# Optimization experiments

Measured on AMD Instinct MI355X. Metric: run time of the kernel, lower is better.

Reference implementation:

```python
import jax, jax.numpy as jnp
import numpy as np

N = 30000
E = 480000
F_IN = 100
HID = 64
HEADS = 4
NCLS = 47
HC = HEADS * HID  # 256
NEG_SLOPE = 0.2
BN_EPS = 1e-5


def setup_inputs() -> dict:
    key = jax.random.key(0)
    ks = jax.random.split(key, 32)
    s = 0.1
    inp = {
        'x': jax.random.normal(ks[0], (N, F_IN), jnp.float32),
        'edge_index': jax.random.randint(ks[1], (2, E), 0, N, jnp.int32),
        # layer 0: GATConv(F_IN -> HID, heads, concat=True)
        'w0': jax.random.normal(ks[2], (F_IN, HC), jnp.float32) * s,
        'as0': jax.random.normal(ks[3], (HEADS, HID), jnp.float32) * s,
        'ad0': jax.random.normal(ks[4], (HEADS, HID), jnp.float32) * s,
        'b0': jnp.zeros((HC,), jnp.float32),
        'sw0': jax.random.normal(ks[5], (F_IN, HC), jnp.float32) * s,
        'sb0': jnp.zeros((HC,), jnp.float32),
        'g0': jnp.ones((HC,), jnp.float32),
        'be0': jnp.zeros((HC,), jnp.float32),
        # layer 1: GATConv(HC -> HID, heads, concat=True)
        'w1': jax.random.normal(ks[6], (HC, HC), jnp.float32) * s,
        'as1': jax.random.normal(ks[7], (HEADS, HID), jnp.float32) * s,
        'ad1': jax.random.normal(ks[8], (HEADS, HID), jnp.float32) * s,
        'b1': jnp.zeros((HC,), jnp.float32),
        'sw1': jax.random.normal(ks[9], (HC, HC), jnp.float32) * s,
        'sb1': jnp.zeros((HC,), jnp.float32),
        'g1': jnp.ones((HC,), jnp.float32),
        'be1': jnp.zeros((HC,), jnp.float32),
        # layer 2: GATConv(HC -> NCLS, heads, concat=False)
        'w2': jax.random.normal(ks[10], (HC, HEADS * NCLS), jnp.float32) * s,
        'as2': jax.random.normal(ks[11], (HEADS, NCLS), jnp.float32) * s,
        'ad2': jax.random.normal(ks[12], (HEADS, NCLS), jnp.float32) * s,
        'b2': jnp.zeros((NCLS,), jnp.float32),
        'sw2': jax.random.normal(ks[13], (HC, NCLS), jnp.float32) * s,
        'sb2': jnp.zeros((NCLS,), jnp.float32),
    }
    return inp


def gat_conv(x, src, dst, W, a_src, a_dst, bias, heads, out_ch, concat):
    # shared linear for src/dst (PyG GATConv with int in_channels)
    h = (x @ W).reshape(N, heads, out_ch)           # [N,H,C]
    al_s = jnp.sum(h * a_src, axis=-1)              # [N,H]
    al_d = jnp.sum(h * a_dst, axis=-1)              # [N,H]
    e = jax.nn.leaky_relu(al_s[src] + al_d[dst], NEG_SLOPE)  # [E,H]
    # segment (per-destination) softmax
    m = jax.ops.segment_max(e, dst, num_segments=N)
    e = jnp.exp(e - m[dst])
    den = jax.ops.segment_sum(e, dst, num_segments=N)
    alpha = e / (den[dst] + 1e-16)                  # [E,H]
    msg = h[src] * alpha[:, :, None]                # [E,H,C]
    out = jax.ops.segment_sum(msg, dst, num_segments=N)  # [N,H,C]
    out = out.reshape(N, heads * out_ch) if concat else out.mean(axis=1)
    return out + bias


def batch_norm(x, gamma, beta):
    mu = jnp.mean(x, axis=0)
    var = jnp.var(x, axis=0)
    return gamma * (x - mu) * jax.lax.rsqrt(var + BN_EPS) + beta


def reference(x, edge_index, w0, as0, ad0, b0, sw0, sb0, g0, be0,
              w1, as1, ad1, b1, sw1, sb1, g1, be1,
              w2, as2, ad2, b2, sw2, sb2):
    src, dst = edge_index[0], edge_index[1]
    # layer 0
    h = gat_conv(x, src, dst, w0, as0, ad0, b0, HEADS, HID, True)
    h = h + x @ sw0 + sb0
    h = jax.nn.elu(batch_norm(h, g0, be0))
    # layer 1
    h2 = gat_conv(h, src, dst, w1, as1, ad1, b1, HEADS, HID, True)
    h2 = h2 + h @ sw1 + sb1
    h2 = jax.nn.elu(batch_norm(h2, g1, be1))
    # layer 2 (concat=False -> mean over heads)
    out = gat_conv(h2, src, dst, w2, as2, ad2, b2, HEADS, NCLS, False)
    out = out + h2 @ sw2 + sb2
    return jax.nn.log_softmax(out, axis=-1)
```

## Files before the change

### kernel.cpp

```cpp
#include <hip/hip_runtime.h>
#include <math.h>

#define NN 30000
#define EE 480000
#define FIN 100
#define NCLS 47
#define NCOPY 16
#define SCAN_B 118

typedef unsigned short ushortt;
typedef __attribute__((ext_vector_type(8))) short bf16x8;
typedef __attribute__((ext_vector_type(8))) unsigned short us8;
typedef __attribute__((ext_vector_type(4))) float f32x4;
typedef __attribute__((ext_vector_type(2))) float f32x2;

__device__ unsigned char g_H8[(size_t)NN * 256];
__device__ ushortt g_Sb[(size_t)NN * 256];
__device__ float   g_S2[(size_t)NN * 48];
__device__ ushortt g_Fb[(size_t)NN * 256];
__device__ ushortt g_Xb[(size_t)NN * 128];
__device__ ushortt g_Wc0[512 * 128];
__device__ ushortt g_Wc1[512 * 256];
__device__ ushortt g_Wc2[235 * 256];
__device__ float g_als[NN * 4];
__device__ float g_ald[NN * 4];
__device__ int   g_rowptr[NN + 1];
__device__ int   g_counts[NN];
__device__ int   g_cur[NN];
__device__ int   g_bsum[128];
__device__ int   g_esrc[EE];
__device__ float g_stat[2 * NCOPY * 512];

__device__ __forceinline__ float wsum(float v) {
#pragma unroll
  for (int o = 32; o > 0; o >>= 1) v += __shfl_xor(v, o, 64);
  return v;
}
__device__ __forceinline__ float lrelu(float x) { return x > 0.f ? x : 0.2f * x; }
__device__ __forceinline__ ushortt f2bf(float f) {
  unsigned int u = __float_as_uint(f);
  unsigned int r = u + 0x7FFF + ((u >> 16) & 1);
  return (ushortt)(r >> 16);
}
__device__ __forceinline__ float bf2f(ushortt u) {
  return __uint_as_float(((unsigned int)u) << 16);
}
__device__ __forceinline__ unsigned int pk4_fp8(float f0, float f1, float f2, float f3) {
  unsigned int r = 0;
  r = __builtin_amdgcn_cvt_pk_fp8_f32(f0, f1, r, false);
  r = __builtin_amdgcn_cvt_pk_fp8_f32(f2, f3, r, true);
  return r;
}
__device__ __forceinline__ int swz(int row, int k) {
  return (k & ~63) | ((((k >> 3) & 7) ^ (row & 7)) << 3) | (k & 7);
}
__device__ __forceinline__ void glds16(const ushortt* gp, ushortt* lp) {
  __builtin_amdgcn_global_load_lds(
      (const __attribute__((address_space(1))) unsigned int*)gp,
      (__attribute__((address_space(3))) unsigned int*)lp, 16, 0, 0);
}

#define CW0 (512 * 128)
#define CW1 (512 * 256)
#define CW2 (235 * 256)
#define STATZ (2 * NCOPY * 512)
__global__ void conv_kernel(const float* __restrict__ w0, const float* __restrict__ sw0,
                            const float* __restrict__ w1, const float* __restrict__ sw1,
                            const float* __restrict__ w2, const float* __restrict__ sw2,
                            const float* __restrict__ x, const int* __restrict__ dst) {
  int i = blockIdx.x * blockDim.x + threadIdx.x;
  if (i < CW0) {
    int m = i >> 7, k = i & 127;
    float v = 0.f;
    if (k < FIN) v = (m < 256) ? w0[k * 256 + m] : sw0[k * 256 + (m - 256)];
    g_Wc0[(m << 7) | swz(m, k)] = f2bf(v);
    return;
  }
  i -= CW0;
  if (i < CW1) {
    int m = i >> 8, k = i & 255;
    float v = (m < 256) ? w1[k * 256 + m] : sw1[k * 256 + (m - 256)];
    g_Wc1[(m << 8) | swz(m, k)] = f2bf(v);
    return;
  }
  i -= CW1;
  if (i < CW2) {
    int m = i >> 8, k = i & 255;
    float v = (m < 188) ? w2[(size_t)k * 188 + m] : sw2[(size_t)k * 47 + (m - 188)];
    g_Wc2[(m << 8) | swz(m, k)] = f2bf(v);
    return;
  }
  i -= CW2;
  if (i < NN * 128) {
    int r = i >> 7, k = i & 127;
    g_Xb[(r << 7) | swz(r, k)] = (k < FIN) ? f2bf(x[r * FIN + k]) : 0;
    return;
  }
  i -= NN * 128;
  if (i < STATZ) {
    g_stat[i] = 0.f;
    return;
  }
  i -= STATZ;
  if (i < EE) atomicAdd(&g_counts[dst[i]], 1);
}

__global__ __launch_bounds__(256) void scan_a() {
  __shared__ int sh[256];
  int t = threadIdx.x;
  int i = blockIdx.x * 256 + t;
  int v = (i < NN) ? g_counts[i] : 0;
  sh[t] = v;
  __syncthreads();
  for (int off = 1; off < 256; off <<= 1) {
    int xv = (t >= off) ? sh[t - off] : 0;
    __syncthreads();
    sh[t] += xv;
    __syncthreads();
  }
  if (i < NN) {
    g_rowptr[i] = sh[t] - v;
    g_counts[i] = 0;
    g_cur[i] = 0;
  }
  if (t == 255) g_bsum[blockIdx.x] = sh[255];
}
__global__ __launch_bounds__(256) void scan_b() {
  __shared__ int sh[4];
  int t = threadIdx.x;
  int b = blockIdx.x;
  int v = (t < b) ? g_bsum[t] : 0;
  float fv = wsum((float)v);
  if ((t & 63) == 0) sh[t >> 6] = (int)fv;
  __syncthreads();
  int off = sh[0] + sh[1] + sh[2] + sh[3];
  int i = b * 256 + t;
  if (i < NN) g_rowptr[i] += off;
  if (i == NN - 1) g_rowptr[NN] = EE;
}
__global__ void scatter_kernel(const int* __restrict__ dst, const int* __restrict__ src) {
  int e = blockIdx.x * blockDim.x + threadIdx.x;
  if (e < EE) {
    int d = dst[e];
    int pos = g_rowptr[d] + atomicAdd(&g_cur[d], 1);
    g_esrc[pos] = src[e];
  }
}

__global__ __launch_bounds__(256) void mfma_gemm(
    const ushortt* __restrict__ A, const ushortt* __restrict__ Wt,
    unsigned char* __restrict__ out8, ushortt* __restrict__ out2b,
    float* __restrict__ out2f,
    int nrows, int Kp, int M, int S, int ld8, int ld2,
    const float* __restrict__ bias2, int pad47,
    const float* __restrict__ a_s, const float* __restrict__ a_d,
    float* __restrict__ alsp, float* __restrict__ aldp) {
  __shared__ __align__(16) ushortt smem[12288];
  ushortt* As = smem;
  ushortt* Ws = smem + 64 * 64;
  float* Ls = (float*)smem;
  int t = threadIdx.x;
  int wave = t >> 6, lane = t & 63;
  int row0 = blockIdx.y * 64, col0 = blockIdx.x * 128;
  int wr = wave >> 1, wc = wave & 1;
  int m16 = lane & 15, q = lane >> 4;
  int rin8 = lane >> 3;
  int koff = (lane & 7) * 8;

  f32x4 acc[2][4];
#pragma unroll
  for (int i = 0; i < 2; i++)
#pragma unroll
    for (int j = 0; j < 4; j++) acc[i][j] = (f32x4){0.f, 0.f, 0.f, 0.f};

  for (int k0 = 0; k0 < Kp; k0 += 64) {
#pragma unroll
    for (int r = 0; r < 2; r++) {
      int lrow = wave * 16 + r * 8;
      int ga = min(row0 + lrow + rin8, nrows - 1);
      glds16(A + (size_t)ga * Kp + k0 + koff, &As[lrow * 64]);
    }
#pragma unroll
    for (int r = 0; r < 4; r++) {
      int lrow = wave * 32 + r * 8;
      int gw = min(col0 + lrow + rin8, M - 1);
      glds16(Wt + (size_t)gw * Kp + k0 + koff, &Ws[lrow * 64]);
    }
    __syncthreads();
#pragma unroll
    for (int c = 0; c < 2; c++) {
      bf16x8 af[2], bf[4];
#pragma unroll
      for (int i = 0; i < 2; i++) {
        int row = wr * 32 + i * 16 + m16;
        int ch = (c * 4 + q) ^ (row & 7);
        af[i] = *(const bf16x8*)(&As[row * 64 + ch * 8]);
      }
#pragma unroll
      for (int i = 0; i < 4; i++) {
        int row = wc * 64 + i * 16 + m16;
        int ch = (c * 4 + q) ^ (row & 7);
        bf[i] = *(const bf16x8*)(&Ws[row * 64 + ch * 8]);
      }
#pragma unroll
      for (int rt = 0; rt < 2; rt++)
#pragma unroll
        for (int ct = 0; ct < 4; ct++)
          acc[rt][ct] = __builtin_amdgcn_mfma_f32_16x16x32_bf16(af[rt], bf[ct], acc[rt][ct], 0, 0, 0);
    }
    __syncthreads();
  }

  bool all1 = (!pad47) && (col0 + 128 <= S);
  bool all2 = (col0 >= S);
  int row8 = t >> 3, seg = t & 7;
#pragma unroll
  for (int p = 0; p < 2; p++) {
    __syncthreads();
    if (wr == p) {
#pragma unroll
      for (int rt = 0; rt < 2; rt++) {
#pragma unroll
        for (int ctt = 0; ctt < 4; ctt++) {
#pragma unroll
          for (int reg = 0; reg < 4; reg++) {
            int rloc = rt * 16 + q * 4 + reg;
            Ls[rloc * 132 + wc * 64 + ctt * 16 + m16] = acc[rt][ctt][reg];
          }
        }
      }
    }
    __syncthreads();
    int grow = row0 + p * 32 + row8;
    if (grow < nrows) {
      const float* lrow = Ls + row8 * 132 + seg * 16;
      int cbase = col0 + seg * 16;
      if (all1) {
        unsigned int q8[4];
#pragma unroll
        for (int kk = 0; kk < 4; kk++)
          q8[kk] = pk4_fp8(lrow[kk * 4], lrow[kk * 4 + 1], lrow[kk * 4 + 2], lrow[kk * 4 + 3]);
        uint4 v8 = {q8[0], q8[1], q8[2], q8[3]};
        *(uint4*)(out8 + (size_t)grow * ld8 + cbase) = v8;
        float s_p = 0.f, d_p = 0.f;
#pragma unroll
        for (int kk = 0; kk < 16; kk++) {
          s_p += lrow[kk] * a_s[cbase + kk];
          d_p += lrow[kk] * a_d[cbase + kk];
        }
        s_p += __shfl_xor(s_p, 1, 64); s_p += __shfl_xor(s_p, 2, 64);
        d_p += __shfl_xor(d_p, 1, 64); d_p += __shfl_xor(d_p, 2, 64);
        if ((seg & 3) == 0) {
          int head = cbase >> 6;
          alsp[grow * 4 + head] = s_p;
          aldp[grow * 4 + head] = d_p;
        }
      } else if (all2) {
        const float* brow = bias2 + (cbase - S);
        ushortt* orow = out2b + (size_t)grow * ld2 + (cbase - S);
        unsigned int pk[8];
#pragma unroll
        for (int kk = 0; kk < 8; kk++) {
          unsigned int lo = f2bf(lrow[kk * 2] + brow[kk * 2]);
          unsigned int hi = f2bf(lrow[kk * 2 + 1] + brow[kk * 2 + 1]);
          pk[kk] = lo | (hi << 16);
        }
        uint4 v0 = {pk[0], pk[1], pk[2], pk[3]};
        uint4 v1 = {pk[4], pk[5], pk[6], pk[7]};
        *(uint4*)(orow) = v0;
        *(uint4*)(orow + 8) = v1;
      } else {
        float pa0 = 0.f, pa1 = 0.f, pd0 = 0.f, pd1 = 0.f;
        int h0 = cbase / 47;
        for (int kk = 0; kk < 16; kk++) {
          int c = cbase + kk;
          if (c >= M) break;
          float v = lrow[kk];
          if (c < S) {
            int hd = c / 47, ch = c - hd * 47;
            int c1 = hd * 48 + ch;
            out8[(size_t)grow * ld8 + c1] =
                (unsigned char)(pk4_fp8(v, 0.f, 0.f, 0.f) & 0xFF);
            if (ch == 46) out8[(size_t)grow * ld8 + c1 + 1] = 0;
            float sw = a_s[hd * 47 + ch], dw = a_d[hd * 47 + ch];
            if (hd == h0) { pa0 += v * sw; pd0 += v * dw; }
            else { pa1 += v * sw; pd1 += v * dw; }
          } else {
            out2f[(size_t)grow * ld2 + (c - S)] = v + bias2[c - S];
          }
        }
        if (pad47 && cbase < S) {
          if (pa0 != 0.f || pd0 != 0.f) {
            atomicAdd(&alsp[grow * 4 + h0], pa0);
            atomicAdd(&aldp[grow * 4 + h0], pd0);
          }
          if ((pa1 != 0.f || pd1 != 0.f) && h0 + 1 < 4) {
            atomicAdd(&alsp[grow * 4 + h0 + 1], pa1);
            atomicAdd(&aldp[grow * 4 + h0 + 1], pd1);
          }
        }
      }
    }
  }
}

__global__ __launch_bounds__(256) void attn_kernel(const unsigned char* __restrict__ H8,
                                                   const float* __restrict__ bias,
                                                   ushortt* __restrict__ Sb,
                                                   float* __restrict__ statp) {
  __shared__ __align__(16) float p_sh[4 * 256];
  __shared__ int s_sh[4 * 64];
  __shared__ float rs_[4 * 256];
  __shared__ float rq_[4 * 256];
  int w = threadIdx.x >> 6, lane = threadIdx.x & 63;
  int n = blockIdx.x * 4 + w;
  float* pw = p_sh + w * 256;
  int* sw_ = s_sh + w * 64;
  int rs = g_rowptr[n], deg = g_rowptr[n + 1] - rs;
  float4 ald = *(const float4*)(g_ald + n * 4);
  int g = lane >> 4;
  int m = lane & 15;
  float den0 = 0, den1 = 0, den2 = 0, den3 = 0;
  float a[16];
#pragma unroll
  for (int k = 0; k < 16; k++) a[k] = 0.f;
  for (int base = 0; base < deg; base += 64) {
    int j = base + lane;
    float p0 = 0, p1 = 0, p2 = 0, p3 = 0;
    int s = 0;
    if (j < deg) {
      s = g_esrc[rs + j];
      float4 av = *(const float4*)(g_als + s * 4);
      p0 = __expf(lrelu(av.x + ald.x)); den0 += p0;
      p1 = __expf(lrelu(av.y + ald.y)); den1 += p1;
      p2 = __expf(lrelu(av.z + ald.z)); den2 += p2;
      p3 = __expf(lrelu(av.w + ald.w)); den3 += p3;
    }
    pw[lane * 4 + 0] = p0; pw[lane * 4 + 1] = p1;
    pw[lane * 4 + 2] = p2; pw[lane * 4 + 3] = p3;
    sw_[lane] = s;
    int cnt = min(64, deg - base);
    for (int jj = 0; jj < cnt; jj += 4) {
      int j4 = jj + g;
      int ss = sw_[j4];
      float p = pw[j4 * 4 + (m >> 2)];
      uint4 hv = *(const uint4*)(H8 + (size_t)ss * 256 + m * 16);
      unsigned int hw[4] = {hv.x, hv.y, hv.z, hv.w};
#pragma unroll
      for (int u = 0; u < 4; u++) {
        f32x2 lo = __builtin_amdgcn_cvt_pk_f32_fp8(hw[u], false);
        f32x2 hi = __builtin_amdgcn_cvt_pk_f32_fp8(hw[u], true);
        a[u * 4 + 0] += p * lo.x;
        a[u * 4 + 1] += p * lo.y;
        a[u * 4 + 2] += p * hi.x;
        a[u * 4 + 3] += p * hi.y;
      }
    }
  }
  den0 = wsum(den0); den1 = wsum(den1); den2 = wsum(den2); den3 = wsum(den3);
#pragma unroll
  for (int k = 0; k < 16; k++) {
    a[k] += __shfl_xor(a[k], 16, 64);
    a[k] += __shfl_xor(a[k], 32, 64);
  }
  int off = g * 4;
  int cb2 = m * 16 + off;
  int head = m >> 2;
  float denq = (head == 0) ? den0 : (head == 1) ? den1 : (head == 2) ? den2 : den3;
  float inv = 1.f / (denq + 1e-16f);
  size_t o = (size_t)n * 256 + cb2;
  ushort4 sv = *(const ushort4*)(Sb + o);
  float4 bv = *(const float4*)(bias + cb2);
  ushort4 ov;
  ov.x = f2bf(a[off + 0] * inv + bv.x + bf2f(sv.x));
  ov.y = f2bf(a[off + 1] * inv + bv.y + bf2f(sv.y));
  ov.z = f2bf(a[off + 2] * inv + bv.z + bf2f(sv.z));
  ov.w = f2bf(a[off + 3] * inv + bv.w + bf2f(sv.w));
  *(ushort4*)(Sb + o) = ov;
  float v0 = bf2f(ov.x), v1 = bf2f(ov.y), v2 = bf2f(ov.z), v3 = bf2f(ov.w);
  int cb = w * 256 + cb2;
  rs_[cb + 0] = v0; rs_[cb + 1] = v1; rs_[cb + 2] = v2; rs_[cb + 3] = v3;
  rq_[cb + 0] = v0 * v0; rq_[cb + 1] = v1 * v1; rq_[cb + 2] = v2 * v2; rq_[cb + 3] = v3 * v3;
  __syncthreads();
  int c = threadIdx.x;
  float s = rs_[c] + rs_[256 + c] + rs_[512 + c] + rs_[768 + c];
  float qq = rq_[c] + rq_[256 + c] + rq_[512 + c] + rq_[768 + c];
  int copy = blockIdx.x & (NCOPY - 1);
  atomicAdd(&statp[copy * 512 + c], s);
  atomicAdd(&statp[copy * 512 + 256 + c], qq);
}

__global__ __launch_bounds__(256) void attn2_kernel(const unsigned char* __restrict__ H8,
                                                    const float* __restrict__ bias,
                                                    const float* __restrict__ S2,
                                                    float* __restrict__ out) {
  __shared__ __align__(16) float p_sh[4 * 256];
  __shared__ int s_sh[4 * 64];
  __shared__ float xh[4][4][48];
  int w = threadIdx.x >> 6, lane = threadIdx.x & 63;
  int n = blockIdx.x * 4 + w;
  float* pw = p_sh + w * 256;
  int* sw_ = s_sh + w * 64;
  int rs = g_rowptr[n], deg = g_rowptr[n + 1] - rs;
  float4 ald = *(const float4*)(g_ald + n * 4);
  int g = lane >> 4;
  int m = lane & 15;
  int mc = min(m, 11);
  int headm = mc / 3;
  float den0 = 0, den1 = 0, den2 = 0, den3 = 0;
  float a[16];
#pragma unroll
  for (int k = 0; k < 16; k++) a[k] = 0.f;
  for (int base = 0; base < deg; base += 64) {
    int j = base + lane;
    float p0 = 0, p1 = 0, p2 = 0, p3 = 0;
    int s = 0;
    if (j < deg) {
      s = g_esrc[rs + j];
      float4 av = *(const float4*)(g_als + s * 4);
      p0 = __expf(lrelu(av.x + ald.x)); den0 += p0;
      p1 = __expf(lrelu(av.y + ald.y)); den1 += p1;
      p2 = __expf(lrelu(av.z + ald.z)); den2 += p2;
      p3 = __expf(lrelu(av.w + ald.w)); den3 += p3;
    }
    pw[lane * 4 + 0] = p0; pw[lane * 4 + 1] = p1;
    pw[lane * 4 + 2] = p2; pw[lane * 4 + 3] = p3;
    sw_[lane] = s;
    int cnt = min(64, deg - base);
    for (int jj = 0; jj < cnt; jj += 4) {
      int j4 = jj + g;
      int ss = sw_[j4];
      float p = (m < 12) ? pw[j4 * 4 + headm] : 0.f;
      uint4 hv = *(const uint4*)(H8 + (size_t)ss * 192 + mc * 16);
      unsigned int hw[4] = {hv.x, hv.y, hv.z, hv.w};
#pragma unroll
      for (int u = 0; u < 4; u++) {
        f32x2 lo = __builtin_amdgcn_cvt_pk_f32_fp8(hw[u], false);
        f32x2 hi = __builtin_amdgcn_cvt_pk_f32_fp8(hw[u], true);
        a[u * 4 + 0] += p * lo.x;
        a[u * 4 + 1] += p * lo.y;
        a[u * 4 + 2] += p * hi.x;
        a[u * 4 + 3] += p * hi.y;
      }
    }
  }
  den0 = wsum(den0); den1 = wsum(den1); den2 = wsum(den2); den3 = wsum(den3);
#pragma unroll
  for (int k = 0; k < 16; k++) {
    a[k] += __shfl_xor(a[k], 16, 64);
    a[k] += __shfl_xor(a[k], 32, 64);
  }
  if (m < 12) {
    int off = g * 4;
    int c192 = m * 16 + off;
    int hd = c192 / 48;
    int chin = c192 - hd * 48;
    float dh = (hd == 0) ? den0 : (hd == 1) ? den1 : (hd == 2) ? den2 : den3;
    float inv = 1.f / (dh + 1e-16f);
    xh[w][hd][chin + 0] = a[off + 0] * inv;
    xh[w][hd][chin + 1] = a[off + 1] * inv;
    xh[w][hd][chin + 2] = a[off + 2] * inv;
    xh[w][hd][chin + 3] = a[off + 3] * inv;
  }
  float v = 0.f;
  if (lane < NCLS)
    v = 0.25f * (xh[w][0][lane] + xh[w][1][lane] + xh[w][2][lane] + xh[w][3][lane]) +
        bias[lane] + S2[(size_t)n * NCLS + lane];
  float mv = (lane < NCLS) ? v : -INFINITY;
#pragma unroll
  for (int o = 32; o > 0; o >>= 1) mv = fmaxf(mv, __shfl_xor(mv, o, 64));
  float ex = (lane < NCLS) ? __expf(v - mv) : 0.f;
  float s = wsum(ex);
  if (lane < NCLS) out[(size_t)n * NCLS + lane] = v - mv - logf(s);
}

__global__ __launch_bounds__(256) void bn_norm_kernel(const ushortt* __restrict__ Sb,
                                                      const float* __restrict__ gamma,
                                                      const float* __restrict__ beta,
                                                      const float* __restrict__ statp,
                                                      float* __restrict__ zs,
                                                      float* __restrict__ zd) {
  __shared__ float sc_sh[256], off_sh[256];
  int t = threadIdx.x;
  float s = 0.f, qq = 0.f;
#pragma unroll
  for (int k = 0; k < NCOPY; k++) {
    s += statp[k * 512 + t];
    qq += statp[k * 512 + 256 + t];
  }
  float mu = s * (1.f / NN);
  float var = qq * (1.f / NN) - mu * mu;
  float rg = rsqrtf(var + 1e-5f) * gamma[t];
  sc_sh[t] = rg;
  off_sh[t] = beta[t] - mu * rg;
  __syncthreads();
  if (zs) {
    for (int i = blockIdx.x * 256 + t; i < NN * 4; i += gridDim.x * 256) {
      zs[i] = 0.f;
      zd[i] = 0.f;
    }
  }
  int rows = (NN + gridDim.x - 1) / gridDim.x;
  int r0 = blockIdx.x * rows, r1 = min(r0 + rows, NN);
  int chunk = t & 31;
  int ro = t >> 5;
  float scv[8], ofv[8];
#pragma unroll
  for (int k = 0; k < 8; k++) {
    scv[k] = sc_sh[chunk * 8 + k];
    ofv[k] = off_sh[chunk * 8 + k];
  }
  for (int r = r0 + ro; r < r1; r += 8) {
    us8 xv = *(const us8*)(Sb + (size_t)r * 256 + chunk * 8);
    us8 yv;
#pragma unroll
    for (int k = 0; k < 8; k++) {
      float v = bf2f((ushortt)xv[k]) * scv[k] + ofv[k];
      v = v > 0.f ? v : (__expf(v) - 1.f);
      yv[k] = f2bf(v);
    }
    int c8 = (chunk & 24) | ((chunk & 7) ^ (r & 7));
    *(us8*)(g_Fb + ((size_t)r << 8) + c8 * 8) = yv;
  }
}

extern "C" void kernel_launch(void* const* d_in, const int* in_sizes, int n_in,
                              void* d_out, int out_size, void* d_ws, size_t ws_size,
                              hipStream_t stream) {
  const float* x = (const float*)d_in[0];
  const int* ei = (const int*)d_in[1];
  const int* src = ei;
  const int* dst = ei + EE;
  const float* w0 = (const float*)d_in[2];
  const float* as0 = (const float*)d_in[3];
  const float* ad0 = (const float*)d_in[4];
  const float* b0 = (const float*)d_in[5];
  const float* sw0 = (const float*)d_in[6];
  const float* sb0 = (const float*)d_in[7];
  const float* gm0 = (const float*)d_in[8];
  const float* be0 = (const float*)d_in[9];
  const float* w1 = (const float*)d_in[10];
  const float* as1 = (const float*)d_in[11];
  const float* ad1 = (const float*)d_in[12];
  const float* b1 = (const float*)d_in[13];
  const float* sw1 = (const float*)d_in[14];
  const float* sb1 = (const float*)d_in[15];
  const float* gm1 = (const float*)d_in[16];
  const float* be1 = (const float*)d_in[17];
  const float* w2 = (const float*)d_in[18];
  const float* as2 = (const float*)d_in[19];
  const float* ad2 = (const float*)d_in[20];
  const float* b2 = (const float*)d_in[21];
  const float* sw2 = (const float*)d_in[22];
  const float* sb2 = (const float*)d_in[23];
  float* out = (float*)d_out;

  ushortt *Sb, *Fb, *Xb, *Wc0, *Wc1, *Wc2;
  unsigned char* H8;
  float *S2, *als, *ald, *stat;
  hipGetSymbolAddress((void**)&H8, HIP_SYMBOL(g_H8));
  hipGetSymbolAddress((void**)&Sb, HIP_SYMBOL(g_Sb));
  hipGetSymbolAddress((void**)&S2, HIP_SYMBOL(g_S2));
  hipGetSymbolAddress((void**)&Fb, HIP_SYMBOL(g_Fb));
  hipGetSymbolAddress((void**)&Xb, HIP_SYMBOL(g_Xb));
  hipGetSymbolAddress((void**)&Wc0, HIP_SYMBOL(g_Wc0));
  hipGetSymbolAddress((void**)&Wc1, HIP_SYMBOL(g_Wc1));
  hipGetSymbolAddress((void**)&Wc2, HIP_SYMBOL(g_Wc2));
  hipGetSymbolAddress((void**)&als, HIP_SYMBOL(g_als));
  hipGetSymbolAddress((void**)&ald, HIP_SYMBOL(g_ald));
  hipGetSymbolAddress((void**)&stat, HIP_SYMBOL(g_stat));

  const int convN = CW0 + CW1 + CW2 + NN * 128 + STATZ + EE;
  conv_kernel<<<(convN + 255) / 256, 256, 0, stream>>>(w0, sw0, w1, sw1, w2, sw2, x, dst);

  scan_a<<<SCAN_B, 256, 0, stream>>>();
  scan_b<<<SCAN_B, 256, 0, stream>>>();
  scatter_kernel<<<(EE + 255) / 256, 256, 0, stream>>>(dst, src);

  const int gy = (NN + 63) / 64;
  const int ga = NN / 4;

  mfma_gemm<<<dim3(4, gy), 256, 0, stream>>>(Xb, Wc0, H8, Sb, nullptr, NN, 128, 512, 256,
                                             256, 256, sb0, 0, as0, ad0, als, ald);
  attn_kernel<<<ga, 256, 0, stream>>>(H8, b0, Sb, stat);
  bn_norm_kernel<<<480, 256, 0, stream>>>(Sb, gm0, be0, stat, nullptr, nullptr);

  mfma_gemm<<<dim3(4, gy), 256, 0, stream>>>(Fb, Wc1, H8, Sb, nullptr, NN, 256, 512, 256,
                                             256, 256, sb1, 0, as1, ad1, als, ald);
  attn_kernel<<<ga, 256, 0, stream>>>(H8, b1, Sb, stat + NCOPY * 512);
  bn_norm_kernel<<<480, 256, 0, stream>>>(Sb, gm1, be1, stat + NCOPY * 512, als, ald);

  mfma_gemm<<<dim3(2, gy), 256, 0, stream>>>(Fb, Wc2, H8, nullptr, S2, NN, 256, 235, 188,
                                             192, 47, sb2, 1, as2, ad2, als, ald);
  attn2_kernel<<<ga, 256, 0, stream>>>(H8, b2, S2, out);
}
```

Before: 379.1 us.

## Fuse block-offset scan into scatter and give GEMM blocks two row tiles

Drops the separate scan_b launch: each scatter block rescans the 118 block sums in shared memory, writes a separate absolute rowptr array, and adds the block offset when placing edges. The attention kernels read the new absolute rowptr. The GEMM now loops over two 64-row tiles per block, halving the grid in y, to amortize block launch and weight staging. The cost is a redundant small scan in every scatter block and fewer GEMM blocks, hence less parallelism, since weight tiles are still reloaded per row tile.

```diff
diff --git a/kernel.cpp b/kernel.cpp
--- a/kernel.cpp
+++ b/kernel.cpp
@@ -25,6 +25,7 @@
 __device__ float g_als[NN * 4];
 __device__ float g_ald[NN * 4];
 __device__ int   g_rowptr[NN + 1];
+__device__ int   g_rowabs[NN + 1];
 __device__ int   g_counts[NN];
 __device__ int   g_cur[NN];
 __device__ int   g_bsum[128];
@@ -125,24 +126,30 @@
   }
   if (t == 255) g_bsum[blockIdx.x] = sh[255];
 }
-__global__ __launch_bounds__(256) void scan_b() {
-  __shared__ int sh[4];
+__global__ __launch_bounds__(256) void scatter_kernel(const int* __restrict__ dst,
+                                                      const int* __restrict__ src) {
+  __shared__ int sh[128];
+  __shared__ int offs[SCAN_B];
   int t = threadIdx.x;
-  int b = blockIdx.x;
-  int v = (t < b) ? g_bsum[t] : 0;
-  float fv = wsum((float)v);
-  if ((t & 63) == 0) sh[t >> 6] = (int)fv;
+  if (t < 128) sh[t] = (t < SCAN_B) ? g_bsum[t] : 0;
   __syncthreads();
-  int off = sh[0] + sh[1] + sh[2] + sh[3];
-  int i = b * 256 + t;
-  if (i < NN) g_rowptr[i] += off;
-  if (i == NN - 1) g_rowptr[NN] = EE;
-}
-__global__ void scatter_kernel(const int* __restrict__ dst, const int* __restrict__ src) {
-  int e = blockIdx.x * blockDim.x + threadIdx.x;
+  for (int off = 1; off < 128; off <<= 1) {
+    int xv = 0;
+    if (t < 128 && t >= off) xv = sh[t - off];
+    __syncthreads();
+    if (t < 128) sh[t] += xv;
+    __syncthreads();
+  }
+  if (t < SCAN_B) offs[t] = sh[t] - g_bsum[t];
+  __syncthreads();
+  int cb = blockIdx.x % SCAN_B;
+  int ri = cb * 256 + t;
+  if (ri < NN) g_rowabs[ri] = g_rowptr[ri] + offs[cb];
+  if (blockIdx.x == 0 && t == 0) g_rowabs[NN] = EE;
+  int e = blockIdx.x * 256 + t;
   if (e < EE) {
     int d = dst[e];
-    int pos = g_rowptr[d] + atomicAdd(&g_cur[d], 1);
+    int pos = g_rowptr[d] + offs[d >> 8] + atomicAdd(&g_cur[d], 1);
     g_esrc[pos] = src[e];
   }
 }
@@ -161,142 +168,146 @@
   float* Ls = (float*)smem;
   int t = threadIdx.x;
   int wave = t >> 6, lane = t & 63;
-  int row0 = blockIdx.y * 64, col0 = blockIdx.x * 128;
+  int col0 = blockIdx.x * 128;
   int wr = wave >> 1, wc = wave & 1;
   int m16 = lane & 15, q = lane >> 4;
   int rin8 = lane >> 3;
   int koff = (lane & 7) * 8;
-
-  f32x4 acc[2][4];
-#pragma unroll
-  for (int i = 0; i < 2; i++)
-#pragma unroll
-    for (int j = 0; j < 4; j++) acc[i][j] = (f32x4){0.f, 0.f, 0.f, 0.f};
-
-  for (int k0 = 0; k0 < Kp; k0 += 64) {
-#pragma unroll
-    for (int r = 0; r < 2; r++) {
-      int lrow = wave * 16 + r * 8;
-      int ga = min(row0 + lrow + rin8, nrows - 1);
-      glds16(A + (size_t)ga * Kp + k0 + koff, &As[lrow * 64]);
-    }
-#pragma unroll
-    for (int r = 0; r < 4; r++) {
-      int lrow = wave * 32 + r * 8;
-      int gw = min(col0 + lrow + rin8, M - 1);
-      glds16(Wt + (size_t)gw * Kp + k0 + koff, &Ws[lrow * 64]);
-    }
-    __syncthreads();
-#pragma unroll
-    for (int c = 0; c < 2; c++) {
-      bf16x8 af[2], bf[4];
-#pragma unroll
-      for (int i = 0; i < 2; i++) {
-        int row = wr * 32 + i * 16 + m16;
-        int ch = (c * 4 + q) ^ (row & 7);
-        af[i] = *(const bf16x8*)(&As[row * 64 + ch * 8]);
-      }
-#pragma unroll
-      for (int i = 0; i < 4; i++) {
-        int row = wc * 64 + i * 16 + m16;
-        int ch = (c * 4 + q) ^ (row & 7);
-        bf[i] = *(const bf16x8*)(&Ws[row * 64 + ch * 8]);
-      }
-#pragma unroll
-      for (int rt = 0; rt < 2; rt++)
-#pragma unroll
-        for (int ct = 0; ct < 4; ct++)
-          acc[rt][ct] = __builtin_amdgcn_mfma_f32_16x16x32_bf16(af[rt], bf[ct], acc[rt][ct], 0, 0, 0);
-    }
-    __syncthreads();
-  }
-
   bool all1 = (!pad47) && (col0 + 128 <= S);
   bool all2 = (col0 >= S);
   int row8 = t >> 3, seg = t & 7;
-#pragma unroll
-  for (int p = 0; p < 2; p++) {
+
+  for (int rt2 = 0; rt2 < 2; rt2++) {
+    int row0 = (blockIdx.y * 2 + rt2) * 64;
+    f32x4 acc[2][4];
+#pragma unroll
+    for (int i = 0; i < 2; i++)
+#pragma unroll
+      for (int j = 0; j < 4; j++) acc[i][j] = (f32x4){0.f, 0.f, 0.f, 0.f};
     __syncthreads();
-    if (wr == p) {
-#pragma unroll
-      for (int rt = 0; rt < 2; rt++) {
-#pragma unroll
-        for (int ctt = 0; ctt < 4; ctt++) {
-#pragma unroll
-          for (int reg = 0; reg < 4; reg++) {
-            int rloc = rt * 16 + q * 4 + reg;
-            Ls[rloc * 132 + wc * 64 + ctt * 16 + m16] = acc[rt][ctt][reg];
+
+    for (int k0 = 0; k0 < Kp; k0 += 64) {
+#pragma unroll
+      for (int r = 0; r < 2; r++) {
+        int lrow = wave * 16 + r * 8;
+        int ga = min(row0 + lrow + rin8, nrows - 1);
+        glds16(A + (size_t)ga * Kp + k0 + koff, &As[lrow * 64]);
+      }
+#pragma unroll
+      for (int r = 0; r < 4; r++) {
+        int lrow = wave * 32 + r * 8;
+        int gw = min(col0 + lrow + rin8, M - 1);
+        glds16(Wt + (size_t)gw * Kp + k0 + koff, &Ws[lrow * 64]);
+      }
+      __syncthreads();
+#pragma unroll
+      for (int c = 0; c < 2; c++) {
+        bf16x8 af[2], bf[4];
+#pragma unroll
+        for (int i = 0; i < 2; i++) {
+          int row = wr * 32 + i * 16 + m16;
+          int ch = (c * 4 + q) ^ (row & 7);
+          af[i] = *(const bf16x8*)(&As[row * 64 + ch * 8]);
+        }
+#pragma unroll
+        for (int i = 0; i < 4; i++) {
+          int row = wc * 64 + i * 16 + m16;
+          int ch = (c * 4 + q) ^ (row & 7);
+          bf[i] = *(const bf16x8*)(&Ws[row * 64 + ch * 8]);
+        }
+#pragma unroll
+        for (int rt = 0; rt < 2; rt++)
+#pragma unroll
+          for (int ct = 0; ct < 4; ct++)
+            acc[rt][ct] = __builtin_amdgcn_mfma_f32_16x16x32_bf16(af[rt], bf[ct], acc[rt][ct], 0, 0, 0);
+      }
+      __syncthreads();
+    }
+
+#pragma unroll
+    for (int p = 0; p < 2; p++) {
+      __syncthreads();
+      if (wr == p) {
+#pragma unroll
+        for (int rt = 0; rt < 2; rt++) {
+#pragma unroll
+          for (int ctt = 0; ctt < 4; ctt++) {
+#pragma unroll
+            for (int reg = 0; reg < 4; reg++) {
+              int rloc = rt * 16 + q * 4 + reg;
+              Ls[rloc * 132 + wc * 64 + ctt * 16 + m16] = acc[rt][ctt][reg];
+            }
           }
         }
       }
-    }
-    __syncthreads();
-    int grow = row0 + p * 32 + row8;
-    if (grow < nrows) {
-      const float* lrow = Ls + row8 * 132 + seg * 16;
-      int cbase = col0 + seg * 16;
-      if (all1) {
-        unsigned int q8[4];
-#pragma unroll
-        for (int kk = 0; kk < 4; kk++)
-          q8[kk] = pk4_fp8(lrow[kk * 4], lrow[kk * 4 + 1], lrow[kk * 4 + 2], lrow[kk * 4 + 3]);
-        uint4 v8 = {q8[0], q8[1], q8[2], q8[3]};
-        *(uint4*)(out8 + (size_t)grow * ld8 + cbase) = v8;
-        float s_p = 0.f, d_p = 0.f;
-#pragma unroll
-        for (int kk = 0; kk < 16; kk++) {
-          s_p += lrow[kk] * a_s[cbase + kk];
-          d_p += lrow[kk] * a_d[cbase + kk];
-        }
-        s_p += __shfl_xor(s_p, 1, 64); s_p += __shfl_xor(s_p, 2, 64);
-        d_p += __shfl_xor(d_p, 1, 64); d_p += __shfl_xor(d_p, 2, 64);
-        if ((seg & 3) == 0) {
-          int head = cbase >> 6;
-          alsp[grow * 4 + head] = s_p;
-          aldp[grow * 4 + head] = d_p;
-        }
-      } else if (all2) {
-        const float* brow = bias2 + (cbase - S);
-        ushortt* orow = out2b + (size_t)grow * ld2 + (cbase - S);
-        unsigned int pk[8];
-#pragma unroll
-        for (int kk = 0; kk < 8; kk++) {
-          unsigned int lo = f2bf(lrow[kk * 2] + brow[kk * 2]);
-          unsigned int hi = f2bf(lrow[kk * 2 + 1] + brow[kk * 2 + 1]);
-          pk[kk] = lo | (hi << 16);
-        }
-        uint4 v0 = {pk[0], pk[1], pk[2], pk[3]};
-        uint4 v1 = {pk[4], pk[5], pk[6], pk[7]};
-        *(uint4*)(orow) = v0;
-        *(uint4*)(orow + 8) = v1;
-      } else {
-        float pa0 = 0.f, pa1 = 0.f, pd0 = 0.f, pd1 = 0.f;
-        int h0 = cbase / 47;
-        for (int kk = 0; kk < 16; kk++) {
-          int c = cbase + kk;
-          if (c >= M) break;
-          float v = lrow[kk];
-          if (c < S) {
-            int hd = c / 47, ch = c - hd * 47;
-            int c1 = hd * 48 + ch;
-            out8[(size_t)grow * ld8 + c1] =
-                (unsigned char)(pk4_fp8(v, 0.f, 0.f, 0.f) & 0xFF);
-            if (ch == 46) out8[(size_t)grow * ld8 + c1 + 1] = 0;
-            float sw = a_s[hd * 47 + ch], dw = a_d[hd * 47 + ch];
-            if (hd == h0) { pa0 += v * sw; pd0 += v * dw; }
-            else { pa1 += v * sw; pd1 += v * dw; }
-          } else {
-            out2f[(size_t)grow * ld2 + (c - S)] = v + bias2[c - S];
+      __syncthreads();
+      int grow = row0 + p * 32 + row8;
+      if (grow < nrows) {
+        const float* lrow = Ls + row8 * 132 + seg * 16;
+        int cbase = col0 + seg * 16;
+        if (all1) {
+          unsigned int q8[4];
+#pragma unroll
+          for (int kk = 0; kk < 4; kk++)
+            q8[kk] = pk4_fp8(lrow[kk * 4], lrow[kk * 4 + 1], lrow[kk * 4 + 2], lrow[kk * 4 + 3]);
+          uint4 v8 = {q8[0], q8[1], q8[2], q8[3]};
+          *(uint4*)(out8 + (size_t)grow * ld8 + cbase) = v8;
+          float s_p = 0.f, d_p = 0.f;
+#pragma unroll
+          for (int kk = 0; kk < 16; kk++) {
+            s_p += lrow[kk] * a_s[cbase + kk];
+            d_p += lrow[kk] * a_d[cbase + kk];
           }
-        }
-        if (pad47 && cbase < S) {
-          if (pa0 != 0.f || pd0 != 0.f) {
-            atomicAdd(&alsp[grow * 4 + h0], pa0);
-            atomicAdd(&aldp[grow * 4 + h0], pd0);
+          s_p += __shfl_xor(s_p, 1, 64); s_p += __shfl_xor(s_p, 2, 64);
+          d_p += __shfl_xor(d_p, 1, 64); d_p += __shfl_xor(d_p, 2, 64);
+          if ((seg & 3) == 0) {
+            int head = cbase >> 6;
+            alsp[grow * 4 + head] = s_p;
+            aldp[grow * 4 + head] = d_p;
           }
-          if ((pa1 != 0.f || pd1 != 0.f) && h0 + 1 < 4) {
-            atomicAdd(&alsp[grow * 4 + h0 + 1], pa1);
-            atomicAdd(&aldp[grow * 4 + h0 + 1], pd1);
+        } else if (all2) {
+          const float* brow = bias2 + (cbase - S);
+          ushortt* orow = out2b + (size_t)grow * ld2 + (cbase - S);
+          unsigned int pk[8];
+#pragma unroll
+          for (int kk = 0; kk < 8; kk++) {
+            unsigned int lo = f2bf(lrow[kk * 2] + brow[kk * 2]);
+            unsigned int hi = f2bf(lrow[kk * 2 + 1] + brow[kk * 2 + 1]);
+            pk[kk] = lo | (hi << 16);
+          }
+          uint4 v0 = {pk[0], pk[1], pk[2], pk[3]};
+          uint4 v1 = {pk[4], pk[5], pk[6], pk[7]};
+          *(uint4*)(orow) = v0;
+          *(uint4*)(orow + 8) = v1;
+        } else {
+          float pa0 = 0.f, pa1 = 0.f, pd0 = 0.f, pd1 = 0.f;
+          int h0 = cbase / 47;
+          for (int kk = 0; kk < 16; kk++) {
+            int c = cbase + kk;
+            if (c >= M) break;
+            float v = lrow[kk];
+            if (c < S) {
+              int hd = c / 47, ch = c - hd * 47;
+              int c1 = hd * 48 + ch;
+              out8[(size_t)grow * ld8 + c1] =
+                  (unsigned char)(pk4_fp8(v, 0.f, 0.f, 0.f) & 0xFF);
+              if (ch == 46) out8[(size_t)grow * ld8 + c1 + 1] = 0;
+              float sw = a_s[hd * 47 + ch], dw = a_d[hd * 47 + ch];
+              if (hd == h0) { pa0 += v * sw; pd0 += v * dw; }
+              else { pa1 += v * sw; pd1 += v * dw; }
+            } else {
+              out2f[(size_t)grow * ld2 + (c - S)] = v + bias2[c - S];
+            }
+          }
+          if (pad47 && cbase < S) {
+            if (pa0 != 0.f || pd0 != 0.f) {
+              atomicAdd(&alsp[grow * 4 + h0], pa0);
+              atomicAdd(&aldp[grow * 4 + h0], pd0);
+            }
+            if ((pa1 != 0.f || pd1 != 0.f) && h0 + 1 < 4) {
+              atomicAdd(&alsp[grow * 4 + h0 + 1], pa1);
+              atomicAdd(&aldp[grow * 4 + h0 + 1], pd1);
+            }
           }
         }
       }
@@ -316,7 +327,7 @@
   int n = blockIdx.x * 4 + w;
   float* pw = p_sh + w * 256;
   int* sw_ = s_sh + w * 64;
-  int rs = g_rowptr[n], deg = g_rowptr[n + 1] - rs;
+  int rs = g_rowabs[n], deg = g_rowabs[n + 1] - rs;
   float4 ald = *(const float4*)(g_ald + n * 4);
   int g = lane >> 4;
   int m = lane & 15;
@@ -401,7 +412,7 @@
   int n = blockIdx.x * 4 + w;
   float* pw = p_sh + w * 256;
   int* sw_ = s_sh + w * 64;
-  int rs = g_rowptr[n], deg = g_rowptr[n + 1] - rs;
+  int rs = g_rowabs[n], deg = g_rowabs[n + 1] - rs;
   float4 ald = *(const float4*)(g_ald + n * 4);
   int g = lane >> 4;
   int m = lane & 15;
@@ -574,10 +585,9 @@
   conv_kernel<<<(convN + 255) / 256, 256, 0, stream>>>(w0, sw0, w1, sw1, w2, sw2, x, dst);
 
   scan_a<<<SCAN_B, 256, 0, stream>>>();
-  scan_b<<<SCAN_B, 256, 0, stream>>>();
   scatter_kernel<<<(EE + 255) / 256, 256, 0, stream>>>(dst, src);
 
-  const int gy = (NN + 63) / 64;
+  const int gy = (NN + 127) / 128;
   const int ga = NN / 4;
 
   mfma_gemm<<<dim3(4, gy), 256, 0, stream>>>(Xb, Wc0, H8, Sb, nullptr, NN, 128, 512, 256,
```

Result: slower. 402.6 us (+6.2%).
